# Performance work log

Measured on AMD Instinct MI355X. Metric: run time of the kernel, lower is better.

Reference implementation:

```python
import jax, jax.numpy as jnp
import numpy as np

B, C_IN, C_OUT, N, K = 16, 128, 128, 4096, 16


def setup_inputs() -> dict:
    key = jax.random.key(0)
    k1, k2, k3, k4 = jax.random.split(key, 4)
    x = jax.random.normal(k1, (B, C_IN, N, 1), dtype=jnp.float32)
    edge_index = jax.random.randint(k2, (2, B, N, K), 0, N, dtype=jnp.int32)
    # 1x1 conv weight of BasicConv([C_IN, C_OUT], 'relu', None, bias=False)
    W = jax.random.normal(k3, (C_OUT, C_IN), dtype=jnp.float32) * (1.0 / np.sqrt(C_IN))
    # module bias param, initialized to zeros; use random here to exercise the add
    bias = jax.random.normal(k4, (1, C_OUT, 1, 1), dtype=jnp.float32) * 0.01
    return {"x": x, "edge_index": edge_index, "W": W, "bias": bias}


def reference(x, edge_index, W, bias):
    b, _, n, _ = x.shape
    # BasicConv: 1x1 conv (no bias) + ReLU
    h = jax.nn.relu(jnp.einsum('oi,binu->bonu', W, x))  # [B, C_out, N, 1]
    h2 = h[..., 0]                                       # [B, C_out, N]
    # add_self_loops: append self index along neighbor dim
    self_idx = jnp.broadcast_to(jnp.arange(n, dtype=edge_index.dtype)[None, None, :, None],
                                (2, b, n, 1))
    ei = jnp.concatenate([edge_index, self_idx], axis=-1)  # [2, B, N, K+1]
    idx = ei[0]                                            # [B, N, K+1]
    deg = ei.shape[-1]
    norm = 1.0 / deg
    # batched_index_select: gather neighbor features -> [B, C_out, N, K+1]
    x_j = jax.vmap(lambda hb, ib: hb[:, ib])(h2, idx)
    aggr = (x_j * norm).sum(axis=-1, keepdims=True)        # [B, C_out, N, 1]
    return aggr + bias
```

## Files before the change

kernel.cpp:

```cpp
#include <hip/hip_runtime.h>

#define B_    16
#define CIN_  128
#define COUT_ 128
#define N_    4096
#define K_    16

typedef __attribute__((ext_vector_type(8))) short bf16x8;
typedef __attribute__((ext_vector_type(4))) float f32x4;
typedef __attribute__((ext_vector_type(4))) int   i32x4;

__device__ inline unsigned short f2bf(float f) {
  unsigned u = __float_as_uint(f);
  u += 0x7fffu + ((u >> 16) & 1u);
  return (unsigned short)(u >> 16);
}

__device__ int g_bar[8 * 32];

__global__ __launch_bounds__(1024, 4) void fused_k(
    const float* __restrict__ W, const float* __restrict__ x,
    const int* __restrict__ ei, const float* __restrict__ bias,
    float* __restrict__ out, unsigned short* __restrict__ h) {
  __shared__ unsigned short Wl[128 * 136];
  __shared__ __align__(16) unsigned short He[256 * 144];
  const int tid  = threadIdx.x;
  const int l    = blockIdx.x;
  const int slot = l >> 3;
  const int b    = ((l & 7) << 1) | (slot >> 4);
  const int n0   = (slot & 15) * 256;

  const int lane = tid & 63;
  const int w    = tid >> 6;
  const int m    = lane & 15;
  const int quad = lane >> 4;

  const float* xb = x + (size_t)b * CIN_ * N_ + n0 + 16 * w + m;
  float xa[32];
#pragma unroll
  for (int s = 0; s < 4; ++s)
#pragma unroll
    for (int j = 0; j < 8; ++j)
      xa[8 * s + j] = xb[(size_t)(32 * s + 8 * quad + j) * N_];

#pragma unroll
  for (int r = 0; r < 2; ++r) {
    int id  = tid + 1024 * r;
    int co  = id >> 4;
    int seg = id & 15;
    const float4* wp = reinterpret_cast<const float4*>(W + co * CIN_ + 8 * seg);
    float4 v0 = wp[0];
    float4 v1 = wp[1];
    unsigned p0 = (unsigned)f2bf(v0.x) | ((unsigned)f2bf(v0.y) << 16);
    unsigned p1 = (unsigned)f2bf(v0.z) | ((unsigned)f2bf(v0.w) << 16);
    unsigned p2 = (unsigned)f2bf(v1.x) | ((unsigned)f2bf(v1.y) << 16);
    unsigned p3 = (unsigned)f2bf(v1.z) | ((unsigned)f2bf(v1.w) << 16);
    *reinterpret_cast<uint4*>(&Wl[co * 136 + 8 * seg]) =
        make_uint4(p0, p1, p2, p3);
  }
  __syncthreads();

  bf16x8 a[4];
#pragma unroll
  for (int s = 0; s < 4; ++s)
#pragma unroll
    for (int j = 0; j < 8; ++j)
      a[s][j] = (short)f2bf(xa[8 * s + j]);

  const int nrow = 16 * w + 4 * quad;
#pragma unroll
  for (int t = 0; t < 8; ++t) {
    f32x4 c = {0.f, 0.f, 0.f, 0.f};
#pragma unroll
    for (int s = 0; s < 4; ++s) {
      bf16x8 bf = *reinterpret_cast<const bf16x8*>(
          &Wl[(16 * t + m) * 136 + 32 * s + 8 * quad]);
      c = __builtin_amdgcn_mfma_f32_16x16x32_bf16(a[s], bf, c, 0, 0, 0);
    }
    int co = 16 * t + m;
#pragma unroll
    for (int r = 0; r < 4; ++r) {
      float v = c[r] > 0.f ? c[r] : 0.f;
      He[(nrow + r) * 144 + co] = f2bf(v);
    }
  }
  __syncthreads();

  {
    unsigned short* hb = h + ((size_t)b * N_ + n0) * COUT_;
    const int seg = tid & 15;
    const int nr  = tid >> 4;
#pragma unroll
    for (int p = 0; p < 4; ++p) {
      int n = nr + 64 * p;
      uint4 v = *reinterpret_cast<const uint4*>(&He[n * 144 + 8 * seg]);
      *reinterpret_cast<uint4*>(hb + (size_t)n * COUT_ + 8 * seg) = v;
    }
  }

  __syncthreads();
  if (tid == 0) {
    int* cnt = &g_bar[(l & 7) * 32];
    int base = __hip_atomic_fetch_add(cnt, 1, __ATOMIC_RELEASE,
                                      __HIP_MEMORY_SCOPE_AGENT);
    int target = (base & ~31) + 32;
    while (__hip_atomic_load(cnt, __ATOMIC_RELAXED,
                             __HIP_MEMORY_SCOPE_AGENT) < target)
      __builtin_amdgcn_s_sleep(4);
  }
  __syncthreads();

  const int s4    = tid >> 8;
  const int t2    = tid & 255;
  const int rest2 = (l >> 3) + 32 * s4;
  const int b2    = ((l & 7) << 1) | (rest2 >> 6);
  const int n02   = (rest2 & 63) * 64;
  int* idxs = reinterpret_cast<int*>(He) + s4 * (17 * 64);

  {
    int n  = t2 >> 2;
    int kq = t2 & 3;
    i32x4 v = __builtin_nontemporal_load(
        reinterpret_cast<const i32x4*>(ei + ((size_t)b2 * N_ + n02 + n) * K_) + kq);
    idxs[(4 * kq + 0) * 64 + n] = v.x;
    idxs[(4 * kq + 1) * 64 + n] = v.y;
    idxs[(4 * kq + 2) * 64 + n] = v.z;
    idxs[(4 * kq + 3) * 64 + n] = v.w;
    if (t2 < 64) idxs[16 * 64 + t2] = n02 + t2;
  }
  __syncthreads();

  const int q = t2 & 15;
  const int g = t2 >> 4;
  const unsigned short* hb2 = h + (size_t)b2 * N_ * COUT_;

  float acc[4][8];
#pragma unroll
  for (int j = 0; j < 4; ++j)
#pragma unroll
    for (int c = 0; c < 8; ++c) acc[j][c] = 0.f;

#pragma unroll 2
  for (int k = 0; k < 17; ++k) {
    uint4 v[4];
#pragma unroll
    for (int j = 0; j < 4; ++j) {
      int node = idxs[k * 64 + 4 * g + j];
      v[j] = *reinterpret_cast<const uint4*>(hb2 + (size_t)node * COUT_ + 8 * q);
    }
#pragma unroll
    for (int j = 0; j < 4; ++j) {
      acc[j][0] += __uint_as_float(v[j].x << 16);
      acc[j][1] += __uint_as_float(v[j].x & 0xffff0000u);
      acc[j][2] += __uint_as_float(v[j].y << 16);
      acc[j][3] += __uint_as_float(v[j].y & 0xffff0000u);
      acc[j][4] += __uint_as_float(v[j].z << 16);
      acc[j][5] += __uint_as_float(v[j].z & 0xffff0000u);
      acc[j][6] += __uint_as_float(v[j].w << 16);
      acc[j][7] += __uint_as_float(v[j].w & 0xffff0000u);
    }
  }

  const float norm = 1.0f / 17.0f;
  const float4 bv0 = *reinterpret_cast<const float4*>(bias + 8 * q);
  const float4 bv1 = *reinterpret_cast<const float4*>(bias + 8 * q + 4);
  float* ob = out + (size_t)b2 * COUT_ * N_ + n02 + 4 * g;
#pragma unroll
  for (int c = 0; c < 8; ++c) {
    int co = 8 * q + c;
    float bb = (c < 4) ? ((c == 0) ? bv0.x : (c == 1) ? bv0.y : (c == 2) ? bv0.z : bv0.w)
                       : ((c == 4) ? bv1.x : (c == 5) ? bv1.y : (c == 6) ? bv1.z : bv1.w);
    float4 r;
    r.x = acc[0][c] * norm + bb;
    r.y = acc[1][c] * norm + bb;
    r.z = acc[2][c] * norm + bb;
    r.w = acc[3][c] * norm + bb;
    *reinterpret_cast<float4*>(ob + (size_t)co * N_) = r;
  }
}

extern "C" void kernel_launch(void* const* d_in, const int* in_sizes, int n_in,
                              void* d_out, int out_size, void* d_ws, size_t ws_size,
                              hipStream_t stream) {
  const float* x    = (const float*)d_in[0];
  const int*   ei   = (const int*)d_in[1];
  const float* W    = (const float*)d_in[2];
  const float* bias = (const float*)d_in[3];
  float* out = (float*)d_out;
  unsigned short* h = (unsigned short*)d_ws;

  fused_k<<<dim3(256), dim3(1024), 0, stream>>>(W, x, ei, bias, out, h);
}
```

Measured before the change: 120.3 us.

## Double grid to 512 blocks, halve per-block tile, prefetch edge indices before barrier

Doubles the grid to 512 blocks of 1024 threads, each computing a 128-node GEMM tile with warps split across output-channel halves. The gather phase now gives each thread 2 nodes instead of 4. Edge-index loads are issued before the h store and the grid barrier so their latency overlaps. The intent is more parallelism and occupancy (launch bounds raised to 8) to hide gather latency, at the cost of more blocks in the spin barrier (64 per group), fewer registers per thread, and narrower output stores.

After: 141.3 us. 1.18x slower.

```diff
diff --git a/kernel.cpp b/kernel.cpp
--- a/kernel.cpp
+++ b/kernel.cpp
@@ -18,30 +18,25 @@
 
 __device__ int g_bar[8 * 32];
 
-__global__ __launch_bounds__(1024, 4) void fused_k(
+__global__ __launch_bounds__(1024, 8) void fused_k(
     const float* __restrict__ W, const float* __restrict__ x,
     const int* __restrict__ ei, const float* __restrict__ bias,
     float* __restrict__ out, unsigned short* __restrict__ h) {
   __shared__ unsigned short Wl[128 * 136];
-  __shared__ __align__(16) unsigned short He[256 * 144];
+  __shared__ __align__(16) unsigned short He[128 * 144];
   const int tid  = threadIdx.x;
   const int l    = blockIdx.x;
+  const int j    = l & 7;
   const int slot = l >> 3;
-  const int b    = ((l & 7) << 1) | (slot >> 4);
-  const int n0   = (slot & 15) * 256;
+  const int b    = (j << 1) | (slot >> 5);
+  const int n0   = (slot & 31) * 128;
 
   const int lane = tid & 63;
   const int w    = tid >> 6;
+  const int wn   = w & 7;
+  const int wg   = w >> 3;
   const int m    = lane & 15;
   const int quad = lane >> 4;
-
-  const float* xb = x + (size_t)b * CIN_ * N_ + n0 + 16 * w + m;
-  float xa[32];
-#pragma unroll
-  for (int s = 0; s < 4; ++s)
-#pragma unroll
-    for (int j = 0; j < 8; ++j)
-      xa[8 * s + j] = xb[(size_t)(32 * s + 8 * quad + j) * N_];
 
 #pragma unroll
   for (int r = 0; r < 2; ++r) {
@@ -58,26 +53,28 @@
     *reinterpret_cast<uint4*>(&Wl[co * 136 + 8 * seg]) =
         make_uint4(p0, p1, p2, p3);
   }
-  __syncthreads();
 
+  const float* xb = x + (size_t)b * CIN_ * N_ + n0 + 16 * wn + m;
   bf16x8 a[4];
 #pragma unroll
   for (int s = 0; s < 4; ++s)
 #pragma unroll
-    for (int j = 0; j < 8; ++j)
-      a[s][j] = (short)f2bf(xa[8 * s + j]);
+    for (int t = 0; t < 8; ++t)
+      a[s][t] = (short)f2bf(xb[(size_t)(32 * s + 8 * quad + t) * N_]);
 
-  const int nrow = 16 * w + 4 * quad;
+  __syncthreads();
+
+  const int nrow = 16 * wn + 4 * quad;
 #pragma unroll
-  for (int t = 0; t < 8; ++t) {
+  for (int t = 0; t < 4; ++t) {
     f32x4 c = {0.f, 0.f, 0.f, 0.f};
 #pragma unroll
     for (int s = 0; s < 4; ++s) {
       bf16x8 bf = *reinterpret_cast<const bf16x8*>(
-          &Wl[(16 * t + m) * 136 + 32 * s + 8 * quad]);
+          &Wl[(64 * wg + 16 * t + m) * 136 + 32 * s + 8 * quad]);
       c = __builtin_amdgcn_mfma_f32_16x16x32_bf16(a[s], bf, c, 0, 0, 0);
     }
-    int co = 16 * t + m;
+    int co = 64 * wg + 16 * t + m;
 #pragma unroll
     for (int r = 0; r < 4; ++r) {
       float v = c[r] > 0.f ? c[r] : 0.f;
@@ -86,47 +83,49 @@
   }
   __syncthreads();
 
+  const int s4    = tid >> 9;
+  const int t2    = tid & 511;
+  const int rest2 = slot + 64 * s4;
+  const int b2    = (j << 1) | (rest2 >> 6);
+  const int n02   = (rest2 & 63) * 64;
+  i32x4 eiv = {0, 0, 0, 0};
+  if (t2 < 256)
+    eiv = __builtin_nontemporal_load(
+        reinterpret_cast<const i32x4*>(ei + ((size_t)b2 * N_ + n02 + (t2 >> 2)) * K_) +
+        (t2 & 3));
+
   {
     unsigned short* hb = h + ((size_t)b * N_ + n0) * COUT_;
     const int seg = tid & 15;
     const int nr  = tid >> 4;
 #pragma unroll
-    for (int p = 0; p < 4; ++p) {
+    for (int p = 0; p < 2; ++p) {
       int n = nr + 64 * p;
       uint4 v = *reinterpret_cast<const uint4*>(&He[n * 144 + 8 * seg]);
       *reinterpret_cast<uint4*>(hb + (size_t)n * COUT_ + 8 * seg) = v;
     }
   }
+  __syncthreads();
 
-  __syncthreads();
+  int* idxs = reinterpret_cast<int*>(He) + s4 * (17 * 64);
+  if (t2 < 256) {
+    int n  = t2 >> 2;
+    int kq = t2 & 3;
+    idxs[(4 * kq + 0) * 64 + n] = eiv.x;
+    idxs[(4 * kq + 1) * 64 + n] = eiv.y;
+    idxs[(4 * kq + 2) * 64 + n] = eiv.z;
+    idxs[(4 * kq + 3) * 64 + n] = eiv.w;
+  }
+  if (t2 < 64) idxs[16 * 64 + t2] = n02 + t2;
+
   if (tid == 0) {
-    int* cnt = &g_bar[(l & 7) * 32];
+    int* cnt = &g_bar[j * 32];
     int base = __hip_atomic_fetch_add(cnt, 1, __ATOMIC_RELEASE,
                                       __HIP_MEMORY_SCOPE_AGENT);
-    int target = (base & ~31) + 32;
+    int target = (base & ~63) + 64;
     while (__hip_atomic_load(cnt, __ATOMIC_RELAXED,
                              __HIP_MEMORY_SCOPE_AGENT) < target)
       __builtin_amdgcn_s_sleep(4);
-  }
-  __syncthreads();
-
-  const int s4    = tid >> 8;
-  const int t2    = tid & 255;
-  const int rest2 = (l >> 3) + 32 * s4;
-  const int b2    = ((l & 7) << 1) | (rest2 >> 6);
-  const int n02   = (rest2 & 63) * 64;
-  int* idxs = reinterpret_cast<int*>(He) + s4 * (17 * 64);
-
-  {
-    int n  = t2 >> 2;
-    int kq = t2 & 3;
-    i32x4 v = __builtin_nontemporal_load(
-        reinterpret_cast<const i32x4*>(ei + ((size_t)b2 * N_ + n02 + n) * K_) + kq);
-    idxs[(4 * kq + 0) * 64 + n] = v.x;
-    idxs[(4 * kq + 1) * 64 + n] = v.y;
-    idxs[(4 * kq + 2) * 64 + n] = v.z;
-    idxs[(4 * kq + 3) * 64 + n] = v.w;
-    if (t2 < 64) idxs[16 * 64 + t2] = n02 + t2;
   }
   __syncthreads();
 
@@ -134,48 +133,46 @@
   const int g = t2 >> 4;
   const unsigned short* hb2 = h + (size_t)b2 * N_ * COUT_;
 
-  float acc[4][8];
+  float acc[2][8];
 #pragma unroll
-  for (int j = 0; j < 4; ++j)
+  for (int jj = 0; jj < 2; ++jj)
 #pragma unroll
-    for (int c = 0; c < 8; ++c) acc[j][c] = 0.f;
+    for (int c = 0; c < 8; ++c) acc[jj][c] = 0.f;
 
 #pragma unroll 2
   for (int k = 0; k < 17; ++k) {
-    uint4 v[4];
+    uint4 v[2];
 #pragma unroll
-    for (int j = 0; j < 4; ++j) {
-      int node = idxs[k * 64 + 4 * g + j];
-      v[j] = *reinterpret_cast<const uint4*>(hb2 + (size_t)node * COUT_ + 8 * q);
+    for (int jj = 0; jj < 2; ++jj) {
+      int node = idxs[k * 64 + 2 * g + jj];
+      v[jj] = *reinterpret_cast<const uint4*>(hb2 + (size_t)node * COUT_ + 8 * q);
     }
 #pragma unroll
-    for (int j = 0; j < 4; ++j) {
-      acc[j][0] += __uint_as_float(v[j].x << 16);
-      acc[j][1] += __uint_as_float(v[j].x & 0xffff0000u);
-      acc[j][2] += __uint_as_float(v[j].y << 16);
-      acc[j][3] += __uint_as_float(v[j].y & 0xffff0000u);
-      acc[j][4] += __uint_as_float(v[j].z << 16);
-      acc[j][5] += __uint_as_float(v[j].z & 0xffff0000u);
-      acc[j][6] += __uint_as_float(v[j].w << 16);
-      acc[j][7] += __uint_as_float(v[j].w & 0xffff0000u);
+    for (int jj = 0; jj < 2; ++jj) {
+      acc[jj][0] += __uint_as_float(v[jj].x << 16);
+      acc[jj][1] += __uint_as_float(v[jj].x & 0xffff0000u);
+      acc[jj][2] += __uint_as_float(v[jj].y << 16);
+      acc[jj][3] += __uint_as_float(v[jj].y & 0xffff0000u);
+      acc[jj][4] += __uint_as_float(v[jj].z << 16);
+      acc[jj][5] += __uint_as_float(v[jj].z & 0xffff0000u);
+      acc[jj][6] += __uint_as_float(v[jj].w << 16);
+      acc[jj][7] += __uint_as_float(v[jj].w & 0xffff0000u);
     }
   }
 
   const float norm = 1.0f / 17.0f;
   const float4 bv0 = *reinterpret_cast<const float4*>(bias + 8 * q);
   const float4 bv1 = *reinterpret_cast<const float4*>(bias + 8 * q + 4);
-  float* ob = out + (size_t)b2 * COUT_ * N_ + n02 + 4 * g;
+  float* ob = out + (size_t)b2 * COUT_ * N_ + n02 + 2 * g;
 #pragma unroll
   for (int c = 0; c < 8; ++c) {
     int co = 8 * q + c;
     float bb = (c < 4) ? ((c == 0) ? bv0.x : (c == 1) ? bv0.y : (c == 2) ? bv0.z : bv0.w)
                        : ((c == 4) ? bv1.x : (c == 5) ? bv1.y : (c == 6) ? bv1.z : bv1.w);
-    float4 r;
+    float2 r;
     r.x = acc[0][c] * norm + bb;
     r.y = acc[1][c] * norm + bb;
-    r.z = acc[2][c] * norm + bb;
-    r.w = acc[3][c] * norm + bb;
-    *reinterpret_cast<float4*>(ob + (size_t)co * N_) = r;
+    *reinterpret_cast<float2*>(ob + (size_t)co * N_) = r;
   }
 }
 
@@ -189,5 +186,5 @@
   float* out = (float*)d_out;
   unsigned short* h = (unsigned short*)d_ws;
 
-  fused_k<<<dim3(256), dim3(1024), 0, stream>>>(W, x, ei, bias, out, h);
+  fused_k<<<dim3(512), dim3(1024), 0, stream>>>(W, x, ei, bias, out, h);
 }
```
